# Performance work log

Hardware: AMD Instinct MI355X
Metric: run time of the kernel (lower is better)

The kernel has to match this reference:

```python
import jax, jax.numpy as jnp
import numpy as np

STATE_DIM, ACTION_DIM, HIDDEN_DIM = 512, 64, 2048
INPUT_DIM = STATE_DIM + ACTION_DIM + 1  # 577
BATCH = 4096


def setup_inputs() -> dict:
    key = jax.random.key(0)
    ks = jax.random.split(key, 12)
    sc_x = 1.0 / np.sqrt(INPUT_DIM)
    sc_h = 1.0 / np.sqrt(HIDDEN_DIM)
    return {
        "s": jax.random.normal(ks[0], (BATCH, STATE_DIM), jnp.float32),
        "a_prev": jax.random.normal(ks[1], (BATCH, ACTION_DIM), jnp.float32),
        "r_prev": jax.random.normal(ks[2], (BATCH, 1), jnp.float32),
        "h": jnp.zeros((HIDDEN_DIM,), jnp.float32),
        "c": jnp.zeros((HIDDEN_DIM,), jnp.float32),
        # Fused gate weights: columns ordered [i, f, g(c-tilde), o]
        "Wx": jax.random.uniform(ks[3], (INPUT_DIM, 4 * HIDDEN_DIM), jnp.float32, -sc_x, sc_x),
        "Wh": jax.random.uniform(ks[4], (HIDDEN_DIM, 4 * HIDDEN_DIM), jnp.float32, -sc_h, sc_h),
        "bh": jax.random.uniform(ks[5], (4 * HIDDEN_DIM,), jnp.float32, -sc_h, sc_h),
        "Wa": jax.random.uniform(ks[6], (HIDDEN_DIM, ACTION_DIM), jnp.float32, -sc_h, sc_h),
        "ba": jax.random.uniform(ks[7], (ACTION_DIM,), jnp.float32, -sc_h, sc_h),
        "Wv": jax.random.uniform(ks[8], (HIDDEN_DIM, 1), jnp.float32, -sc_h, sc_h),
        "bv": jax.random.uniform(ks[9], (1,), jnp.float32, -sc_h, sc_h),
    }


def reference(s, a_prev, r_prev, h, c, Wx, Wh, bh, Wa, ba, Wv, bv):
    # x: [B, input_dim]
    x = jnp.concatenate([s, a_prev, r_prev], axis=1)
    # Two fused GEMMs replace the 8 separate small linears (same math).
    z = x @ Wx + h @ Wh + bh          # [B, 4H]
    zi, zf, zg, zo = jnp.split(z, 4, axis=-1)
    i = jax.nn.sigmoid(zi)
    f = jax.nn.sigmoid(zf)
    c_new = f * c + i * jnp.tanh(zg)  # [B, H] (c broadcast over batch)
    o = jax.nn.sigmoid(zo)
    h_new = o * jnp.tanh(c_new)       # [B, H]
    probs = jax.nn.softmax(h_new @ Wa + ba, axis=1)  # [B, A]
    v = h_new @ Wv + bv               # [B, 1]
    return (probs, v)
```

## Files before the change

kernel.cpp:

```cpp
#include <hip/hip_runtime.h>
#include <hip/hip_bf16.h>

#define BATCH   4096
#define SDIM    512
#define ADIM    64
#define IDIM    577
#define KP2     576
#define NKT64   9
#define HDIM    2048
#define ZDIM    8192
#define BUFE    (128 * 64)

typedef __attribute__((ext_vector_type(8))) __bf16 bf16x8;
typedef __attribute__((ext_vector_type(4))) float  accx4;

__global__ __launch_bounds__(256) void setup_kernel(
    const float* __restrict__ s, const float* __restrict__ a_prev,
    const float* __restrict__ h,
    const float* __restrict__ wx, const float* __restrict__ wh,
    const float* __restrict__ wa,
    __hip_bfloat16* __restrict__ xb, __hip_bfloat16* __restrict__ wxt,
    __hip_bfloat16* __restrict__ waT, float* __restrict__ zh_w)
{
    __shared__ float stile[64 * 65];
    const int bid = blockIdx.x;
    const int t = threadIdx.x;

    if (bid < 1152) {
        const int kt2 = bid >> 7;
        const int nt  = bid & 127;
        const int c4  = t & 15;
        const int rr  = t >> 4;
#pragma unroll
        for (int i = 0; i < 4; ++i) {
            const int r = rr + i * 16;
            const int k = kt2 * 64 + r;
            float4 v =
                *(const float4*)(wx + (size_t)k * ZDIM + nt * 64 + c4 * 4);
            *(float4*)(stile + r * 65 + c4 * 4) = v;
        }
        __syncthreads();
        const int ch = t & 7;
#pragma unroll
        for (int i = 0; i < 2; ++i) {
            const int nr = (t >> 3) + i * 32;
            bf16x8 w8;
#pragma unroll
            for (int j = 0; j < 8; ++j)
                w8[j] = (__bf16)stile[(ch * 8 + j) * 65 + nr];
            *(bf16x8*)(wxt + (size_t)(nt * 64 + nr) * KP2 + kt2 * 64 + ch * 8)
                = w8;
        }
    } else if (bid < 1664) {
        const int zb = bid - 1152;
        const int nb = zb & 31, ky = zb >> 5;
        const int n  = nb * 256 + t;
        const float* hp  = h + ky * 128;
        const float* whp = wh + (size_t)ky * 128 * ZDIM + n;
        float p = 0.0f;
#pragma unroll 32
        for (int kk = 0; kk < 128; ++kk)
            p = fmaf(hp[kk], whp[(size_t)kk * ZDIM], p);
        zh_w[ky * ZDIM + n] = p;
    } else if (bid < 5760) {
        const int row = bid - 1664;
        const float* srow = s + (size_t)row * SDIM;
        const float* arow = a_prev + (size_t)row * ADIM;
        __hip_bfloat16* xrow = xb + (size_t)row * KP2;
        for (int c = t; c < KP2; c += 256) {
            const float v = (c < SDIM) ? srow[c] : arow[c - SDIM];
            xrow[c] = __float2bfloat16(v);
        }
    } else {
        const int wb = bid - 5760;
        const int kt = wb >> 1, at = wb & 1;
        const int c  = t & 31, r0 = t >> 5;
#pragma unroll
        for (int i = 0; i < 4; ++i) {
            int r = r0 + i * 8;
            stile[r * 33 + c] = wa[(size_t)(kt * 32 + r) * ADIM + at * 32 + c];
        }
        __syncthreads();
#pragma unroll
        for (int i = 0; i < 4; ++i) {
            int r = r0 + i * 8;
            waT[(size_t)(at * 32 + r) * HDIM + kt * 32 + c] =
                __float2bfloat16(stile[c * 33 + r]);
        }
    }
}

__device__ __forceinline__ float rcp_f(float x) {
    return __builtin_amdgcn_rcpf(x);
}
__device__ __forceinline__ float sigmoid_f(float x) {
    return rcp_f(1.0f + __expf(-x));
}
__device__ __forceinline__ float tanh_f(float x) {
    return 1.0f - 2.0f * rcp_f(1.0f + __expf(2.0f * x));
}

__global__ __launch_bounds__(256, 2) void lstm_gemm(
    const __hip_bfloat16* __restrict__ xb,
    const __hip_bfloat16* __restrict__ wxt,
    const float* __restrict__ zh_w,
    const float* __restrict__ bh,
    const float* __restrict__ cvec,
    const float* __restrict__ wx,
    const float* __restrict__ r_prev,
    __hip_bfloat16* __restrict__ hout)
{
    __shared__ __bf16 smA[2 * BUFE];
    __shared__ __bf16 smB[2 * BUFE];
    const int t    = threadIdx.x;
    const int lane = t & 63;
    const int wid  = t >> 6;
    const int m0   = blockIdx.x * 128;
    const int n0   = blockIdx.y * 32;
    const int wm   = wid >> 1, wn = wid & 1;
    const int fl15 = lane & 15;
    const int fhi  = lane >> 4;

    accx4 acc[4][4] = {};

    const int srow = lane >> 3;
    const int slot = lane & 7;
    const int cch  = slot ^ srow;
    const __bf16* gA[4]; const __bf16* gB[4]; int lofs[4];
#pragma unroll
    for (int i = 0; i < 4; ++i) {
        const int r = wid * 32 + i * 8 + srow;
        gA[i] = (const __bf16*)xb + (size_t)(m0 + r) * KP2 + cch * 8;
        const int g = r >> 5, nn = r & 31;
        gB[i] = (const __bf16*)wxt +
                (size_t)(g * HDIM + n0 + nn) * KP2 + cch * 8;
        lofs[i] = (wid * 32 + i * 8) * 64;
    }

    auto stage = [&](int tile, int p) {
        const int ko = tile * 64;
        const int po = p * BUFE;
#pragma unroll
        for (int i = 0; i < 4; ++i) {
            __builtin_amdgcn_global_load_lds(
                (const __attribute__((address_space(1))) void*)(gA[i] + ko),
                (__attribute__((address_space(3))) void*)(smA + po + lofs[i]),
                16, 0, 0);
            __builtin_amdgcn_global_load_lds(
                (const __attribute__((address_space(1))) void*)(gB[i] + ko),
                (__attribute__((address_space(3))) void*)(smB + po + lofs[i]),
                16, 0, 0);
        }
    };

    auto compute = [&](int p) {
        const int po = p * BUFE;
#pragma unroll
        for (int hf = 0; hf < 2; ++hf) {
            const int ck = hf * 4 + fhi;
            const int sl = (ck ^ (fl15 & 7)) * 8;
            bf16x8 af[4], bfr[4];
#pragma unroll
            for (int rt = 0; rt < 4; ++rt)
                af[rt] = *(const bf16x8*)(smA + po +
                    (wm * 64 + rt * 16 + fl15) * 64 + sl);
#pragma unroll
            for (int g = 0; g < 4; ++g)
                bfr[g] = *(const bf16x8*)(smB + po +
                    (g * 32 + wn * 16 + fl15) * 64 + sl);
#pragma unroll
            for (int g = 0; g < 4; ++g)
#pragma unroll
                for (int rt = 0; rt < 4; ++rt)
                    acc[g][rt] = __builtin_amdgcn_mfma_f32_16x16x32_bf16(
                        af[rt], bfr[g], acc[g][rt], 0, 0, 0);
        }
    };

    stage(0, 0);
    __syncthreads();
#pragma unroll
    for (int kt = 0; kt < NKT64 - 1; ++kt) {
        stage(kt + 1, (kt + 1) & 1);
        compute(kt & 1);
        __syncthreads();
    }
    compute((NKT64 - 1) & 1);

    const int colg = n0 + wn * 16 + fl15;
    float zsum[4], wxr[4];
#pragma unroll
    for (int g = 0; g < 4; ++g) {
        float z = bh[g * HDIM + colg];
#pragma unroll
        for (int j = 0; j < 16; ++j)
            z += zh_w[j * ZDIM + g * HDIM + colg];
        zsum[g] = z;
        wxr[g] = wx[(size_t)576 * ZDIM + g * HDIM + colg];
    }
    const float cv = cvec[colg];
#pragma unroll
    for (int rt = 0; rt < 4; ++rt) {
#pragma unroll
        for (int r = 0; r < 4; ++r) {
            const int row = m0 + wm * 64 + rt * 16 + (fhi << 2) + r;
            const float rv = r_prev[row];
            const float zi = acc[0][rt][r] + zsum[0] + rv * wxr[0];
            const float zf = acc[1][rt][r] + zsum[1] + rv * wxr[1];
            const float zg = acc[2][rt][r] + zsum[2] + rv * wxr[2];
            const float zo = acc[3][rt][r] + zsum[3] + rv * wxr[3];
            const float cn = sigmoid_f(zf) * cv + sigmoid_f(zi) * tanh_f(zg);
            const float hn = sigmoid_f(zo) * tanh_f(cn);
            hout[(size_t)row * HDIM + colg] = __float2bfloat16(hn);
        }
    }
}

__global__ __launch_bounds__(512) void head_kernel(
    const __hip_bfloat16* __restrict__ hnew,
    const __hip_bfloat16* __restrict__ waT,
    const float* __restrict__ wv,
    const float* __restrict__ ba, const float* __restrict__ bv,
    float* __restrict__ probs, float* __restrict__ vout)
{
    __shared__ float lg[8][16][68];
    __shared__ float vpart[8][16];
    const int t    = threadIdx.x;
    const int lane = t & 63;
    const int w    = t >> 6;
    const int r0   = blockIdx.x * 16;
    const int fl15 = lane & 15, fhi = lane >> 4;
    const int k0   = w * 256;

    const __bf16* arow = (const __bf16*)hnew +
        (size_t)(r0 + fl15) * HDIM + k0 + fhi * 8;
    const __bf16* brow = (const __bf16*)waT +
        (size_t)fl15 * HDIM + k0 + fhi * 8;
    const float* wvp = wv + k0 + fhi * 8;

    accx4 acc[4] = {};
    float va0 = 0.f, va1 = 0.f;
#pragma unroll
    for (int kk = 0; kk < 256; kk += 32) {
        bf16x8 af = *(const bf16x8*)(arow + kk);
#pragma unroll
        for (int a = 0; a < 4; ++a) {
            bf16x8 bf = *(const bf16x8*)(brow + (size_t)a * 16 * HDIM + kk);
            acc[a] = __builtin_amdgcn_mfma_f32_16x16x32_bf16(
                af, bf, acc[a], 0, 0, 0);
        }
#pragma unroll
        for (int j = 0; j < 4; ++j) {
            va0 = fmaf((float)af[j],     wvp[kk + j],     va0);
            va1 = fmaf((float)af[j + 4], wvp[kk + j + 4], va1);
        }
    }
#pragma unroll
    for (int a = 0; a < 4; ++a)
#pragma unroll
        for (int r = 0; r < 4; ++r)
            lg[w][fhi * 4 + r][a * 16 + fl15] = acc[a][r];
    float va = va0 + va1;
    va += __shfl_xor(va, 16);
    va += __shfl_xor(va, 32);
    if (lane < 16) vpart[w][lane] = va;
    __syncthreads();

    const float bav = ba[lane];
#pragma unroll
    for (int i = 0; i < 2; ++i) {
        const int row = w * 2 + i;
        float logit = bav;
#pragma unroll
        for (int p = 0; p < 8; ++p)
            logit += lg[p][row][lane];
        float m = logit;
#pragma unroll
        for (int mask = 32; mask >= 1; mask >>= 1)
            m = fmaxf(m, __shfl_xor(m, mask));
        const float e = __expf(logit - m);
        float ssum = e;
#pragma unroll
        for (int mask = 32; mask >= 1; mask >>= 1)
            ssum += __shfl_xor(ssum, mask);
        probs[(size_t)(r0 + row) * 64 + lane] = e / ssum;
    }
    if (t < 16) {
        float v = bv[0];
#pragma unroll
        for (int p = 0; p < 8; ++p)
            v += vpart[p][t];
        vout[r0 + t] = v;
    }
}

extern "C" void kernel_launch(void* const* d_in, const int* in_sizes, int n_in,
                              void* d_out, int out_size, void* d_ws,
                              size_t ws_size, hipStream_t stream)
{
    const float* s      = (const float*)d_in[0];
    const float* a_prev = (const float*)d_in[1];
    const float* r_prev = (const float*)d_in[2];
    const float* h      = (const float*)d_in[3];
    const float* c      = (const float*)d_in[4];
    const float* Wx     = (const float*)d_in[5];
    const float* Wh     = (const float*)d_in[6];
    const float* bh     = (const float*)d_in[7];
    const float* Wa     = (const float*)d_in[8];
    const float* ba     = (const float*)d_in[9];
    const float* Wv     = (const float*)d_in[10];
    const float* bv     = (const float*)d_in[11];

    float* out   = (float*)d_out;
    float* probs = out;
    float* vout  = out + (size_t)BATCH * ADIM;

    char* ws = (char*)d_ws;
    __hip_bfloat16* xb   = (__hip_bfloat16*)ws;
    __hip_bfloat16* wxt  = (__hip_bfloat16*)(ws + 4718592);
    __hip_bfloat16* waT  = (__hip_bfloat16*)(ws + 14155776);
    float* zh_w          = (float*)(ws + 14417920);
    __hip_bfloat16* hnew = (__hip_bfloat16*)(ws + 14942208);

    setup_kernel<<<5888, 256, 0, stream>>>(
        s, a_prev, h, Wx, Wh, Wa, xb, wxt, waT, zh_w);
    lstm_gemm<<<dim3(BATCH / 128, HDIM / 32), 256, 0, stream>>>(
        xb, wxt, zh_w, bh, c, Wx, r_prev, hnew);
    head_kernel<<<BATCH / 16, 512, 0, stream>>>(
        hnew, waT, Wv, ba, bv, probs, vout);
}
```

Baseline: 204.6 us.

## Fuse policy/value head into LSTM GEMM via last-block atomic counter

Result: slower. 485.5 us (+137.3%).

```diff
diff --git a/kernel.cpp b/kernel.cpp
--- a/kernel.cpp
+++ b/kernel.cpp
@@ -108,10 +108,16 @@
     const float* __restrict__ cvec,
     const float* __restrict__ wx,
     const float* __restrict__ r_prev,
-    __hip_bfloat16* __restrict__ hout)
+    __hip_bfloat16* __restrict__ hout,
+    const __hip_bfloat16* __restrict__ waT,
+    const float* __restrict__ wv,
+    const float* __restrict__ ba, const float* __restrict__ bv,
+    float* __restrict__ probs, float* __restrict__ vout,
+    int* __restrict__ mcount)
 {
     __shared__ __bf16 smA[2 * BUFE];
     __shared__ __bf16 smB[2 * BUFE];
+    __shared__ int lastflag;
     const int t    = threadIdx.x;
     const int lane = t & 63;
     const int wid  = t >> 6;
@@ -214,83 +220,72 @@
             hout[(size_t)row * HDIM + colg] = __float2bfloat16(hn);
         }
     }
-}
-
-__global__ __launch_bounds__(512) void head_kernel(
-    const __hip_bfloat16* __restrict__ hnew,
-    const __hip_bfloat16* __restrict__ waT,
-    const float* __restrict__ wv,
-    const float* __restrict__ ba, const float* __restrict__ bv,
-    float* __restrict__ probs, float* __restrict__ vout)
-{
-    __shared__ float lg[8][16][68];
-    __shared__ float vpart[8][16];
-    const int t    = threadIdx.x;
-    const int lane = t & 63;
-    const int w    = t >> 6;
-    const int r0   = blockIdx.x * 16;
-    const int fl15 = lane & 15, fhi = lane >> 4;
-    const int k0   = w * 256;
-
-    const __bf16* arow = (const __bf16*)hnew +
-        (size_t)(r0 + fl15) * HDIM + k0 + fhi * 8;
-    const __bf16* brow = (const __bf16*)waT +
-        (size_t)fl15 * HDIM + k0 + fhi * 8;
-    const float* wvp = wv + k0 + fhi * 8;
-
-    accx4 acc[4] = {};
-    float va0 = 0.f, va1 = 0.f;
-#pragma unroll
-    for (int kk = 0; kk < 256; kk += 32) {
-        bf16x8 af = *(const bf16x8*)(arow + kk);
-#pragma unroll
-        for (int a = 0; a < 4; ++a) {
-            bf16x8 bf = *(const bf16x8*)(brow + (size_t)a * 16 * HDIM + kk);
-            acc[a] = __builtin_amdgcn_mfma_f32_16x16x32_bf16(
-                af, bf, acc[a], 0, 0, 0);
-        }
-#pragma unroll
-        for (int j = 0; j < 4; ++j) {
-            va0 = fmaf((float)af[j],     wvp[kk + j],     va0);
-            va1 = fmaf((float)af[j + 4], wvp[kk + j + 4], va1);
-        }
-    }
-#pragma unroll
-    for (int a = 0; a < 4; ++a)
-#pragma unroll
-        for (int r = 0; r < 4; ++r)
-            lg[w][fhi * 4 + r][a * 16 + fl15] = acc[a][r];
-    float va = va0 + va1;
-    va += __shfl_xor(va, 16);
-    va += __shfl_xor(va, 32);
-    if (lane < 16) vpart[w][lane] = va;
+
+    __threadfence();
+    if (t == 0) {
+        const int old = atomicAdd(&mcount[blockIdx.x], 1);
+        lastflag = (old == 63);
+    }
     __syncthreads();
-
-    const float bav = ba[lane];
-#pragma unroll
-    for (int i = 0; i < 2; ++i) {
-        const int row = w * 2 + i;
-        float logit = bav;
-#pragma unroll
-        for (int p = 0; p < 8; ++p)
-            logit += lg[p][row][lane];
-        float m = logit;
-#pragma unroll
-        for (int mask = 32; mask >= 1; mask >>= 1)
-            m = fmaxf(m, __shfl_xor(m, mask));
-        const float e = __expf(logit - m);
-        float ssum = e;
-#pragma unroll
-        for (int mask = 32; mask >= 1; mask >>= 1)
-            ssum += __shfl_xor(ssum, mask);
-        probs[(size_t)(r0 + row) * 64 + lane] = e / ssum;
-    }
-    if (t < 16) {
-        float v = bv[0];
-#pragma unroll
-        for (int p = 0; p < 8; ++p)
-            v += vpart[p][t];
-        vout[r0 + t] = v;
+    if (!lastflag) return;
+    __threadfence();
+
+    const float bav0 = ba[fl15];
+    const float bav1 = ba[16 + fl15];
+    const float bav2 = ba[32 + fl15];
+    const float bav3 = ba[48 + fl15];
+    const float bvv  = bv[0];
+#pragma unroll
+    for (int rg = 0; rg < 2; ++rg) {
+        const int r0h = m0 + wid * 32 + rg * 16;
+        const __bf16* arow = (const __bf16*)hout +
+            (size_t)(r0h + fl15) * HDIM + fhi * 8;
+        const float* wvp = wv + fhi * 8;
+        accx4 ha[4] = {};
+        float va0 = 0.f, va1 = 0.f;
+#pragma unroll 4
+        for (int kk = 0; kk < HDIM; kk += 32) {
+            bf16x8 af = *(const bf16x8*)(arow + kk);
+#pragma unroll
+            for (int a = 0; a < 4; ++a) {
+                bf16x8 bf = *(const bf16x8*)((const __bf16*)waT +
+                    (size_t)(a * 16 + fl15) * HDIM + fhi * 8 + kk);
+                ha[a] = __builtin_amdgcn_mfma_f32_16x16x32_bf16(
+                    af, bf, ha[a], 0, 0, 0);
+            }
+#pragma unroll
+            for (int j = 0; j < 4; ++j) {
+                va0 = fmaf((float)af[j],     wvp[kk + j],     va0);
+                va1 = fmaf((float)af[j + 4], wvp[kk + j + 4], va1);
+            }
+        }
+#pragma unroll
+        for (int r = 0; r < 4; ++r) {
+            const float l0 = ha[0][r] + bav0;
+            const float l1 = ha[1][r] + bav1;
+            const float l2 = ha[2][r] + bav2;
+            const float l3 = ha[3][r] + bav3;
+            float m = fmaxf(fmaxf(l0, l1), fmaxf(l2, l3));
+#pragma unroll
+            for (int mask = 1; mask <= 8; mask <<= 1)
+                m = fmaxf(m, __shfl_xor(m, mask));
+            const float e0 = __expf(l0 - m), e1 = __expf(l1 - m);
+            const float e2 = __expf(l2 - m), e3 = __expf(l3 - m);
+            float ssum = (e0 + e1) + (e2 + e3);
+#pragma unroll
+            for (int mask = 1; mask <= 8; mask <<= 1)
+                ssum += __shfl_xor(ssum, mask);
+            const float inv = rcp_f(ssum);
+            float* prow = probs + (size_t)(r0h + fhi * 4 + r) * 64 + fl15;
+            prow[0]  = e0 * inv;
+            prow[16] = e1 * inv;
+            prow[32] = e2 * inv;
+            prow[48] = e3 * inv;
+        }
+        float va = va0 + va1;
+        va += __shfl_xor(va, 16);
+        va += __shfl_xor(va, 32);
+        if (lane < 16) vout[r0h + lane] = va + bvv;
     }
 }
 
@@ -321,11 +316,12 @@
     __hip_bfloat16* waT  = (__hip_bfloat16*)(ws + 14155776);
     float* zh_w          = (float*)(ws + 14417920);
     __hip_bfloat16* hnew = (__hip_bfloat16*)(ws + 14942208);
+    int* mcount          = (int*)(ws + 31719424);
 
     setup_kernel<<<5888, 256, 0, stream>>>(
         s, a_prev, h, Wx, Wh, Wa, xb, wxt, waT, zh_w);
+    hipMemsetAsync(mcount, 0, 32 * sizeof(int), stream);
     lstm_gemm<<<dim3(BATCH / 128, HDIM / 32), 256, 0, stream>>>(
-        xb, wxt, zh_w, bh, c, Wx, r_prev, hnew);
-    head_kernel<<<BATCH / 16, 512, 0, stream>>>(
-        hnew, waT, Wv, ba, bv, probs, vout);
-}
+        xb, wxt, zh_w, bh, c, Wx, r_prev, hnew,
+        waT, Wv, ba, bv, probs, vout, mcount);
+}
```
